# Kernel tuning notes

Measured on AMD Instinct MI355X. Metric: run time of the kernel, lower is better.

## Reference

```python
import jax, jax.numpy as jnp
import numpy as np

H = 512          # hidden_size
B, S, L = 32, 2048, 2
D = 2 * H        # encoder output / hidden feature dim


def setup_inputs() -> dict:
    key = jax.random.key(0)
    ks = jax.random.split(key, 9)
    lim1 = 1.0 / np.sqrt(D)
    limv = 1.0 / np.sqrt(H)
    return {
        "hidden": jax.random.normal(ks[0], (L, B, D), jnp.float32),
        "encoder_outputs": jax.random.normal(ks[1], (B, S, D), jnp.float32),
        "mask": jax.random.randint(ks[2], (B, S), 0, 2, jnp.int32),
        "W1_w": jax.random.uniform(ks[3], (H, D), jnp.float32, -lim1, lim1),
        "W1_b": jax.random.uniform(ks[4], (H,), jnp.float32, -lim1, lim1),
        "W2_w": jax.random.uniform(ks[5], (H, D), jnp.float32, -lim1, lim1),
        "W2_b": jax.random.uniform(ks[6], (H,), jnp.float32, -lim1, lim1),
        "V_w": jax.random.uniform(ks[7], (1, H), jnp.float32, -limv, limv),
        "V_b": jax.random.uniform(ks[8], (1,), jnp.float32, -limv, limv),
    }


def reference(hidden, encoder_outputs, mask, W1_w, W1_b, W2_w, W2_b, V_w, V_b):
    # query: last layer hidden state, broadcast over sequence -> [B, 1, D]
    query = hidden[-1][:, None, :]
    # W1(enc) + W2(query): [B, S, H]
    proj = (jnp.einsum('bsd,hd->bsh', encoder_outputs, W1_w) + W1_b
            + jnp.einsum('bqd,hd->bqh', query, W2_w) + W2_b)
    # V projection -> scores [B, S]
    score = jnp.einsum('bsh,h->bs', jnp.tanh(proj), V_w[0]) + V_b[0]
    score = jnp.where(mask == 0, jnp.float32(-1e9), score)
    attn_weights = jax.nn.softmax(score, axis=1)          # [B, S]
    context = jnp.einsum('bs,bsd->bd', attn_weights, encoder_outputs)  # [B, D]
    return context, attn_weights
```

## Files before the change

kernel.cpp:

```cpp
#include <hip/hip_runtime.h>
#include <hip/hip_bf16.h>

#define B_ 32
#define S_ 2048
#define D_ 1024
#define H_ 512
#define M_ (B_*S_)
#define BM 128
#define BN 128
#define BK 64

typedef __attribute__((ext_vector_type(8))) short short8;
typedef __attribute__((ext_vector_type(4))) float f32x4;

__device__ __forceinline__ unsigned short f2bf(float f){
  unsigned u = __builtin_bit_cast(unsigned, f);
  u += 0x7FFFu + ((u>>16)&1u);
  return (unsigned short)(u>>16);
}

__device__ __forceinline__ int swz(int row, int kshort){
  return row*BK + ((kshort & 56) ^ ((row&7)<<3)) + (kshort & 7);
}

__global__ __launch_bounds__(256) void convw_kernel(
    const float* __restrict__ W1, unsigned short* __restrict__ W1s){
  int tid = blockIdx.x*256 + threadIdx.x;
  int n = tid*8;
  int h = n >> 10;
  int k = n & 1023;
  int bn = h >> 7, row = h & 127;
  int kt = k >> 6, kk = k & 63;
  float4 lo = *(const float4*)(W1 + n);
  float4 hi = *(const float4*)(W1 + n + 4);
  short8 r;
  r[0]=(short)f2bf(lo.x); r[1]=(short)f2bf(lo.y); r[2]=(short)f2bf(lo.z); r[3]=(short)f2bf(lo.w);
  r[4]=(short)f2bf(hi.x); r[5]=(short)f2bf(hi.y); r[6]=(short)f2bf(hi.z); r[7]=(short)f2bf(hi.w);
  *(short8*)&W1s[(bn*16 + kt)*(BN*BK) + swz(row, kk)] = r;
}

__global__ __launch_bounds__(256) void qbias_kernel(
    const float* __restrict__ hidden, const float* __restrict__ W2,
    const float* __restrict__ W1b, const float* __restrict__ W2b,
    float* __restrict__ qb){
  int b = blockIdx.x, h0 = blockIdx.y*64;
  int wave = threadIdx.x>>6, lane = threadIdx.x&63;
  const float* q = hidden + (size_t)(B_ + b)*D_;
  for (int i=0;i<16;i++){
    int h = h0 + wave*16 + i;
    const float* w = W2 + (size_t)h*D_;
    float s = 0.f;
    #pragma unroll
    for (int it=0; it<4; ++it){
      int d = it*256 + lane*4;
      const float4 qq = *(const float4*)(q+d);
      const float4 ww = *(const float4*)(w+d);
      s += qq.x*ww.x + qq.y*ww.y + qq.z*ww.z + qq.w*ww.w;
    }
    #pragma unroll
    for (int off=1; off<64; off<<=1) s += __shfl_xor(s, off);
    if (lane==0) qb[b*H_ + h] = s + W1b[h] + W2b[h];
  }
}

__global__ __launch_bounds__(256, 2) void score_gemm(
    const float* __restrict__ enc, const unsigned short* __restrict__ W1s,
    const float* __restrict__ qb, const float* __restrict__ Vw,
    float* __restrict__ score_p){
  const int id  = blockIdx.x;
  const int xcd = id & 7;
  const int j   = id >> 3;
  const int bm  = xcd*64 + (j >> 2);
  const int bn  = j & 3;
  const int m0 = bm*BM, h0 = bn*BN;
  const int tid = threadIdx.x, lane = tid&63, wave = tid>>6;
  const int wm = (wave>>1)*64, wn = (wave&1)*64;

  __shared__ __align__(16) unsigned short As[BM*BK];
  __shared__ __align__(16) unsigned short Bs[BN*BK];

  f32x4 acc[4][4];
  #pragma unroll
  for (int i=0;i<4;i++)
    #pragma unroll
    for (int j2=0;j2<4;j2++)
      acc[i][j2] = (f32x4)(0.f);

  const int arow = tid>>3, akc = (tid&7)*8;

  float4 aLo[4], aHi[4];
  #pragma unroll
  for (int i=0;i<4;i++){
    int c = tid + i*256;
    int row = c>>3, kc = (c&7)*8;
    const float4* pa = (const float4*)(enc + (size_t)(m0+row)*D_ + kc);
    aLo[i]=pa[0]; aHi[i]=pa[1];
  }

  for (int kt=0; kt<16; ++kt){
    __builtin_amdgcn_s_barrier();
    __builtin_amdgcn_sched_barrier(0);
    const unsigned short* bsrc = W1s + (bn*16 + kt)*(BN*BK);
    #pragma unroll
    for (int i=0;i<4;i++){
      __builtin_amdgcn_global_load_lds(
        (const __attribute__((address_space(1))) unsigned int*)(bsrc + i*2048 + tid*8),
        (__attribute__((address_space(3))) unsigned int*)&Bs[i*2048 + tid*8],
        16, 0, 0);
    }
    __builtin_amdgcn_sched_barrier(0);
    #pragma unroll
    for (int i=0;i<4;i++){
      int c = tid + i*256;
      int row = c>>3, kc = (c&7)*8;
      short8 av;
      av[0]=(short)f2bf(aLo[i].x); av[1]=(short)f2bf(aLo[i].y);
      av[2]=(short)f2bf(aLo[i].z); av[3]=(short)f2bf(aLo[i].w);
      av[4]=(short)f2bf(aHi[i].x); av[5]=(short)f2bf(aHi[i].y);
      av[6]=(short)f2bf(aHi[i].z); av[7]=(short)f2bf(aHi[i].w);
      *(short8*)&As[swz(row, kc)] = av;
    }
    if (kt < 15){
      const int kk1 = (kt+1)*BK;
      #pragma unroll
      for (int i=0;i<4;i++){
        int c = tid + i*256;
        int row = c>>3, kc = (c&7)*8;
        const float4* pa = (const float4*)(enc + (size_t)(m0+row)*D_ + kk1 + kc);
        aLo[i]=pa[0]; aHi[i]=pa[1];
      }
      __builtin_amdgcn_sched_barrier(0);
      asm volatile("s_waitcnt vmcnt(8) lgkmcnt(0)" ::: "memory");
    } else {
      __builtin_amdgcn_sched_barrier(0);
      asm volatile("s_waitcnt vmcnt(0) lgkmcnt(0)" ::: "memory");
    }
    __builtin_amdgcn_s_barrier();
    __builtin_amdgcn_sched_barrier(0);
    #pragma unroll
    for (int kh=0; kh<2; ++kh){
      const int kb = kh*32 + (lane>>4)*8;
      short8 af[4], bf[4];
      #pragma unroll
      for (int mi=0;mi<4;mi++){
        int row = wm + mi*16 + (lane&15);
        af[mi] = *(const short8*)&As[swz(row, kb)];
      }
      #pragma unroll
      for (int ni=0;ni<4;ni++){
        int row = wn + ni*16 + (lane&15);
        bf[ni] = *(const short8*)&Bs[swz(row, kb)];
      }
      #pragma unroll
      for (int mi=0;mi<4;mi++)
        #pragma unroll
        for (int ni=0;ni<4;ni++)
          acc[mi][ni] = __builtin_amdgcn_mfma_f32_16x16x32_bf16(af[mi], bf[ni], acc[mi][ni], 0,0,0);
    }
  }

  const int bidx = m0 >> 11;
  float qv[4], vwv[4];
  #pragma unroll
  for (int ni=0;ni<4;ni++){
    int h = h0 + wn + ni*16 + (lane&15);
    qv[ni]  = qb[bidx*H_ + h];
    vwv[ni] = Vw[h];
  }
  __shared__ float psum[4][BM];
  #pragma unroll
  for (int mi=0;mi<4;mi++){
    #pragma unroll
    for (int r=0;r<4;r++){
      float s = 0.f;
      #pragma unroll
      for (int ni=0;ni<4;ni++) s += tanhf(acc[mi][ni][r] + qv[ni]) * vwv[ni];
      s += __shfl_xor(s,1); s += __shfl_xor(s,2);
      s += __shfl_xor(s,4); s += __shfl_xor(s,8);
      if ((lane&15)==0){
        int m = wm + mi*16 + ((lane>>4)<<2) + r;
        psum[wave][m] = s;
      }
    }
  }
  __syncthreads();
  if (tid < BM){
    int w0 = (tid>>6)*2;
    score_p[(size_t)bn*M_ + m0 + tid] = psum[w0][tid] + psum[w0+1][tid];
  }
}

__global__ __launch_bounds__(256) void softmax_kernel(
    const float* __restrict__ score_p, const int* __restrict__ mask,
    float* __restrict__ attn){
  int b = blockIdx.x, tid = threadIdx.x;
  int wave = tid>>6, lane = tid&63;
  __shared__ float red[8];
  float v[8];
  float mx = -1e30f;
  #pragma unroll
  for (int i=0;i<8;i++){
    int idx = b*S_ + tid + i*256;
    float sc = score_p[idx] + score_p[M_+idx] + score_p[2*M_+idx] + score_p[3*M_+idx];
    v[i] = (mask[idx]==0) ? -1e9f : sc;
    mx = fmaxf(mx, v[i]);
  }
  #pragma unroll
  for (int off=1; off<64; off<<=1) mx = fmaxf(mx, __shfl_xor(mx, off));
  if (lane==0) red[wave] = mx;
  __syncthreads();
  mx = fmaxf(fmaxf(red[0],red[1]), fmaxf(red[2],red[3]));
  float sum = 0.f;
  #pragma unroll
  for (int i=0;i<8;i++){ v[i] = __expf(v[i]-mx); sum += v[i]; }
  #pragma unroll
  for (int off=1; off<64; off<<=1) sum += __shfl_xor(sum, off);
  if (lane==0) red[4+wave] = sum;
  __syncthreads();
  float inv = 1.f/(red[4]+red[5]+red[6]+red[7]);
  #pragma unroll
  for (int i=0;i<8;i++) attn[b*S_ + tid + i*256] = v[i]*inv;
}

__global__ __launch_bounds__(256) void context_kernel(
    const float* __restrict__ enc, const float* __restrict__ attn,
    float* __restrict__ ctx){
  int b = blockIdx.x, sc = blockIdx.y;
  int s0 = sc*64;
  int d4 = threadIdx.x*4;
  const float* ep = enc + ((size_t)b*S_ + s0)*D_ + d4;
  const float* ap = attn + b*S_ + s0;
  float4 a0 = make_float4(0.f,0.f,0.f,0.f);
  float4 a1 = make_float4(0.f,0.f,0.f,0.f);
  #pragma unroll 4
  for (int i=0;i<64;i+=2){
    float w0 = ap[i], w1 = ap[i+1];
    float4 e0 = *(const float4*)(ep + (size_t)i*D_);
    float4 e1 = *(const float4*)(ep + (size_t)(i+1)*D_);
    a0.x = fmaf(w0, e0.x, a0.x); a0.y = fmaf(w0, e0.y, a0.y);
    a0.z = fmaf(w0, e0.z, a0.z); a0.w = fmaf(w0, e0.w, a0.w);
    a1.x = fmaf(w1, e1.x, a1.x); a1.y = fmaf(w1, e1.y, a1.y);
    a1.z = fmaf(w1, e1.z, a1.z); a1.w = fmaf(w1, e1.w, a1.w);
  }
  float* o = ctx + b*D_ + d4;
  atomicAdd(o+0, a0.x+a1.x); atomicAdd(o+1, a0.y+a1.y);
  atomicAdd(o+2, a0.z+a1.z); atomicAdd(o+3, a0.w+a1.w);
}

extern "C" void kernel_launch(void* const* d_in, const int* in_sizes, int n_in,
                              void* d_out, int out_size, void* d_ws, size_t ws_size,
                              hipStream_t stream){
  const float* hidden = (const float*)d_in[0];
  const float* enc    = (const float*)d_in[1];
  const int*   mask   = (const int*)d_in[2];
  const float* W1w    = (const float*)d_in[3];
  const float* W1b    = (const float*)d_in[4];
  const float* W2w    = (const float*)d_in[5];
  const float* W2b    = (const float*)d_in[6];
  const float* Vw     = (const float*)d_in[7];
  float* out = (float*)d_out;

  float* qb           = (float*)d_ws;
  float* score_p      = qb + B_*H_;
  unsigned short* W1s = (unsigned short*)(score_p + 4*M_);

  hipMemsetAsync(out, 0, (size_t)B_*D_*sizeof(float), stream);

  convw_kernel  <<<H_*D_/8/256,     256, 0, stream>>>(W1w, W1s);
  qbias_kernel  <<<dim3(B_, H_/64), 256, 0, stream>>>(hidden, W2w, W1b, W2b, qb);
  score_gemm    <<<4*(M_/BM),       256, 0, stream>>>(enc, W1s, qb, Vw, score_p);
  softmax_kernel<<<B_,              256, 0, stream>>>(score_p, mask, out + B_*D_);
  context_kernel<<<dim3(B_, 32),    256, 0, stream>>>(enc, out + B_*D_, out);
}
```

Baseline: 190.3 us.

## Double-buffer score GEMM LDS, use fast tanh, restructure qbias and context kernels

The score GEMM now keeps two LDS buffers for A and B, so the next tile's loads and bf16 conversion overlap MFMA compute with one barrier per k-step instead of two. tanhf is replaced by an exp/rcp formulation to cut epilogue cost. qbias is reorganised so each W2 row is loaded once and reused across all batches, using fewer blocks. The context kernel uses nontemporal vector loads and four accumulators. The costs are double the LDS for the GEMM and slightly lower tanh accuracy.

```diff
diff --git a/kernel.cpp b/kernel.cpp
--- a/kernel.cpp
+++ b/kernel.cpp
@@ -9,6 +9,7 @@
 #define BM 128
 #define BN 128
 #define BK 64
+#define TILE (BM*BK)
 
 typedef __attribute__((ext_vector_type(8))) short short8;
 typedef __attribute__((ext_vector_type(4))) float f32x4;
@@ -17,6 +18,10 @@
   unsigned u = __builtin_bit_cast(unsigned, f);
   u += 0x7FFFu + ((u>>16)&1u);
   return (unsigned short)(u>>16);
+}
+
+__device__ __forceinline__ float fast_tanh(float x){
+  return 1.f - 2.f*__builtin_amdgcn_rcpf(__expf(2.f*x) + 1.f);
 }
 
 __device__ __forceinline__ int swz(int row, int kshort){
@@ -36,30 +41,34 @@
   short8 r;
   r[0]=(short)f2bf(lo.x); r[1]=(short)f2bf(lo.y); r[2]=(short)f2bf(lo.z); r[3]=(short)f2bf(lo.w);
   r[4]=(short)f2bf(hi.x); r[5]=(short)f2bf(hi.y); r[6]=(short)f2bf(hi.z); r[7]=(short)f2bf(hi.w);
-  *(short8*)&W1s[(bn*16 + kt)*(BN*BK) + swz(row, kk)] = r;
+  *(short8*)&W1s[(bn*16 + kt)*TILE + swz(row, kk)] = r;
 }
 
 __global__ __launch_bounds__(256) void qbias_kernel(
     const float* __restrict__ hidden, const float* __restrict__ W2,
     const float* __restrict__ W1b, const float* __restrict__ W2b,
     float* __restrict__ qb){
-  int b = blockIdx.x, h0 = blockIdx.y*64;
+  int h0 = blockIdx.x*16;
   int wave = threadIdx.x>>6, lane = threadIdx.x&63;
-  const float* q = hidden + (size_t)(B_ + b)*D_;
-  for (int i=0;i<16;i++){
-    int h = h0 + wave*16 + i;
+  for (int r=0;r<4;r++){
+    int h = h0 + wave*4 + r;
     const float* w = W2 + (size_t)h*D_;
-    float s = 0.f;
+    float4 wv[4];
     #pragma unroll
-    for (int it=0; it<4; ++it){
-      int d = it*256 + lane*4;
-      const float4 qq = *(const float4*)(q+d);
-      const float4 ww = *(const float4*)(w+d);
-      s += qq.x*ww.x + qq.y*ww.y + qq.z*ww.z + qq.w*ww.w;
+    for (int it=0;it<4;it++) wv[it] = *(const float4*)(w + it*256 + lane*4);
+    float bias = W1b[h] + W2b[h];
+    for (int b=0;b<B_;b++){
+      const float* q = hidden + (size_t)(B_+b)*D_;
+      float s = 0.f;
+      #pragma unroll
+      for (int it=0;it<4;it++){
+        float4 qq = *(const float4*)(q + it*256 + lane*4);
+        s += qq.x*wv[it].x + qq.y*wv[it].y + qq.z*wv[it].z + qq.w*wv[it].w;
+      }
+      #pragma unroll
+      for (int off=1; off<64; off<<=1) s += __shfl_xor(s, off);
+      if (lane==0) qb[b*H_ + h] = s + bias;
     }
-    #pragma unroll
-    for (int off=1; off<64; off<<=1) s += __shfl_xor(s, off);
-    if (lane==0) qb[b*H_ + h] = s + W1b[h] + W2b[h];
   }
 }
 
@@ -76,8 +85,8 @@
   const int tid = threadIdx.x, lane = tid&63, wave = tid>>6;
   const int wm = (wave>>1)*64, wn = (wave&1)*64;
 
-  __shared__ __align__(16) unsigned short As[BM*BK];
-  __shared__ __align__(16) unsigned short Bs[BN*BK];
+  __shared__ __align__(16) unsigned short As[2][TILE];
+  __shared__ __align__(16) unsigned short Bs[2][TILE];
 
   f32x4 acc[4][4];
   #pragma unroll
@@ -86,78 +95,65 @@
     for (int j2=0;j2<4;j2++)
       acc[i][j2] = (f32x4)(0.f);
 
-  const int arow = tid>>3, akc = (tid&7)*8;
-
   float4 aLo[4], aHi[4];
-  #pragma unroll
-  for (int i=0;i<4;i++){
-    int c = tid + i*256;
-    int row = c>>3, kc = (c&7)*8;
-    const float4* pa = (const float4*)(enc + (size_t)(m0+row)*D_ + kc);
-    aLo[i]=pa[0]; aHi[i]=pa[1];
-  }
-
-  for (int kt=0; kt<16; ++kt){
+
+#define LOAD_A(KT) do{ const int kkx=(KT)*BK; \
+  _Pragma("unroll") for (int i=0;i<4;i++){ \
+    int c=tid+i*256; int row=c>>3, kc=(c&7)*8; \
+    const float4* pa=(const float4*)(enc+(size_t)(m0+row)*D_+kkx+kc); \
+    aLo[i]=pa[0]; aHi[i]=pa[1]; } }while(0)
+
+#define GLD_B(KT,P) do{ const unsigned short* bsrc=W1s+(size_t)(bn*16+(KT))*TILE; \
+  _Pragma("unroll") for (int i=0;i<4;i++){ \
+    __builtin_amdgcn_global_load_lds( \
+      (const __attribute__((address_space(1))) unsigned int*)(bsrc+i*2048+tid*8), \
+      (__attribute__((address_space(3))) unsigned int*)&Bs[P][i*2048+tid*8], 16,0,0); } }while(0)
+
+#define CVT_A(P) do{ \
+  _Pragma("unroll") for (int i=0;i<4;i++){ \
+    int c=tid+i*256; int row=c>>3, kc=(c&7)*8; short8 av; \
+    av[0]=(short)f2bf(aLo[i].x); av[1]=(short)f2bf(aLo[i].y); \
+    av[2]=(short)f2bf(aLo[i].z); av[3]=(short)f2bf(aLo[i].w); \
+    av[4]=(short)f2bf(aHi[i].x); av[5]=(short)f2bf(aHi[i].y); \
+    av[6]=(short)f2bf(aHi[i].z); av[7]=(short)f2bf(aHi[i].w); \
+    *(short8*)&As[P][swz(row,kc)] = av; } }while(0)
+
+#define COMPUTE(P) do{ \
+  _Pragma("unroll") for (int kh=0; kh<2; ++kh){ \
+    const int kb = kh*32 + (lane>>4)*8; \
+    short8 af[4], bf[4]; \
+    _Pragma("unroll") for (int mi=0;mi<4;mi++){ \
+      int row=wm+mi*16+(lane&15); af[mi]=*(const short8*)&As[P][swz(row,kb)]; } \
+    _Pragma("unroll") for (int ni=0;ni<4;ni++){ \
+      int row=wn+ni*16+(lane&15); bf[ni]=*(const short8*)&Bs[P][swz(row,kb)]; } \
+    _Pragma("unroll") for (int mi=0;mi<4;mi++) \
+      _Pragma("unroll") for (int ni=0;ni<4;ni++) \
+        acc[mi][ni]=__builtin_amdgcn_mfma_f32_16x16x32_bf16(af[mi],bf[ni],acc[mi][ni],0,0,0); \
+  } }while(0)
+
+  LOAD_A(0);
+  GLD_B(0,0);
+  CVT_A(0);
+  LOAD_A(1);
+  asm volatile("s_waitcnt vmcnt(8) lgkmcnt(0)" ::: "memory");
+  __builtin_amdgcn_s_barrier();
+
+  #pragma unroll 2
+  for (int kt=0; kt<14; ++kt){
+    const int p = kt&1;
+    GLD_B(kt+1, p^1);
+    CVT_A(p^1);
+    LOAD_A(kt+2);
+    COMPUTE(p);
+    asm volatile("s_waitcnt vmcnt(8) lgkmcnt(0)" ::: "memory");
     __builtin_amdgcn_s_barrier();
-    __builtin_amdgcn_sched_barrier(0);
-    const unsigned short* bsrc = W1s + (bn*16 + kt)*(BN*BK);
-    #pragma unroll
-    for (int i=0;i<4;i++){
-      __builtin_amdgcn_global_load_lds(
-        (const __attribute__((address_space(1))) unsigned int*)(bsrc + i*2048 + tid*8),
-        (__attribute__((address_space(3))) unsigned int*)&Bs[i*2048 + tid*8],
-        16, 0, 0);
-    }
-    __builtin_amdgcn_sched_barrier(0);
-    #pragma unroll
-    for (int i=0;i<4;i++){
-      int c = tid + i*256;
-      int row = c>>3, kc = (c&7)*8;
-      short8 av;
-      av[0]=(short)f2bf(aLo[i].x); av[1]=(short)f2bf(aLo[i].y);
-      av[2]=(short)f2bf(aLo[i].z); av[3]=(short)f2bf(aLo[i].w);
-      av[4]=(short)f2bf(aHi[i].x); av[5]=(short)f2bf(aHi[i].y);
-      av[6]=(short)f2bf(aHi[i].z); av[7]=(short)f2bf(aHi[i].w);
-      *(short8*)&As[swz(row, kc)] = av;
-    }
-    if (kt < 15){
-      const int kk1 = (kt+1)*BK;
-      #pragma unroll
-      for (int i=0;i<4;i++){
-        int c = tid + i*256;
-        int row = c>>3, kc = (c&7)*8;
-        const float4* pa = (const float4*)(enc + (size_t)(m0+row)*D_ + kk1 + kc);
-        aLo[i]=pa[0]; aHi[i]=pa[1];
-      }
-      __builtin_amdgcn_sched_barrier(0);
-      asm volatile("s_waitcnt vmcnt(8) lgkmcnt(0)" ::: "memory");
-    } else {
-      __builtin_amdgcn_sched_barrier(0);
-      asm volatile("s_waitcnt vmcnt(0) lgkmcnt(0)" ::: "memory");
-    }
-    __builtin_amdgcn_s_barrier();
-    __builtin_amdgcn_sched_barrier(0);
-    #pragma unroll
-    for (int kh=0; kh<2; ++kh){
-      const int kb = kh*32 + (lane>>4)*8;
-      short8 af[4], bf[4];
-      #pragma unroll
-      for (int mi=0;mi<4;mi++){
-        int row = wm + mi*16 + (lane&15);
-        af[mi] = *(const short8*)&As[swz(row, kb)];
-      }
-      #pragma unroll
-      for (int ni=0;ni<4;ni++){
-        int row = wn + ni*16 + (lane&15);
-        bf[ni] = *(const short8*)&Bs[swz(row, kb)];
-      }
-      #pragma unroll
-      for (int mi=0;mi<4;mi++)
-        #pragma unroll
-        for (int ni=0;ni<4;ni++)
-          acc[mi][ni] = __builtin_amdgcn_mfma_f32_16x16x32_bf16(af[mi], bf[ni], acc[mi][ni], 0,0,0);
-    }
-  }
+  }
+  GLD_B(15,1);
+  CVT_A(1);
+  COMPUTE(0);
+  asm volatile("s_waitcnt vmcnt(0) lgkmcnt(0)" ::: "memory");
+  __builtin_amdgcn_s_barrier();
+  COMPUTE(1);
 
   const int bidx = m0 >> 11;
   float qv[4], vwv[4];
@@ -174,7 +170,7 @@
     for (int r=0;r<4;r++){
       float s = 0.f;
       #pragma unroll
-      for (int ni=0;ni<4;ni++) s += tanhf(acc[mi][ni][r] + qv[ni]) * vwv[ni];
+      for (int ni=0;ni<4;ni++) s += fast_tanh(acc[mi][ni][r] + qv[ni]) * vwv[ni];
       s += __shfl_xor(s,1); s += __shfl_xor(s,2);
       s += __shfl_xor(s,4); s += __shfl_xor(s,8);
       if ((lane&15)==0){
@@ -230,21 +226,20 @@
   int d4 = threadIdx.x*4;
   const float* ep = enc + ((size_t)b*S_ + s0)*D_ + d4;
   const float* ap = attn + b*S_ + s0;
-  float4 a0 = make_float4(0.f,0.f,0.f,0.f);
-  float4 a1 = make_float4(0.f,0.f,0.f,0.f);
-  #pragma unroll 4
-  for (int i=0;i<64;i+=2){
-    float w0 = ap[i], w1 = ap[i+1];
-    float4 e0 = *(const float4*)(ep + (size_t)i*D_);
-    float4 e1 = *(const float4*)(ep + (size_t)(i+1)*D_);
-    a0.x = fmaf(w0, e0.x, a0.x); a0.y = fmaf(w0, e0.y, a0.y);
-    a0.z = fmaf(w0, e0.z, a0.z); a0.w = fmaf(w0, e0.w, a0.w);
-    a1.x = fmaf(w1, e1.x, a1.x); a1.y = fmaf(w1, e1.y, a1.y);
-    a1.z = fmaf(w1, e1.z, a1.z); a1.w = fmaf(w1, e1.w, a1.w);
-  }
+  f32x4 a0=(f32x4)(0.f), a1=(f32x4)(0.f), a2=(f32x4)(0.f), a3=(f32x4)(0.f);
+  #pragma unroll 2
+  for (int i=0;i<64;i+=4){
+    f32x4 w = *(const f32x4*)(ap + i);
+    f32x4 e0 = __builtin_nontemporal_load((const f32x4*)(ep + (size_t)i*D_));
+    f32x4 e1 = __builtin_nontemporal_load((const f32x4*)(ep + (size_t)(i+1)*D_));
+    f32x4 e2 = __builtin_nontemporal_load((const f32x4*)(ep + (size_t)(i+2)*D_));
+    f32x4 e3 = __builtin_nontemporal_load((const f32x4*)(ep + (size_t)(i+3)*D_));
+    a0 += w[0]*e0; a1 += w[1]*e1; a2 += w[2]*e2; a3 += w[3]*e3;
+  }
+  f32x4 t = (a0+a1) + (a2+a3);
   float* o = ctx + b*D_ + d4;
-  atomicAdd(o+0, a0.x+a1.x); atomicAdd(o+1, a0.y+a1.y);
-  atomicAdd(o+2, a0.z+a1.z); atomicAdd(o+3, a0.w+a1.w);
+  atomicAdd(o+0, t[0]); atomicAdd(o+1, t[1]);
+  atomicAdd(o+2, t[2]); atomicAdd(o+3, t[3]);
 }
 
 extern "C" void kernel_launch(void* const* d_in, const int* in_sizes, int n_in,
@@ -266,9 +261,9 @@
 
   hipMemsetAsync(out, 0, (size_t)B_*D_*sizeof(float), stream);
 
-  convw_kernel  <<<H_*D_/8/256,     256, 0, stream>>>(W1w, W1s);
-  qbias_kernel  <<<dim3(B_, H_/64), 256, 0, stream>>>(hidden, W2w, W1b, W2b, qb);
-  score_gemm    <<<4*(M_/BM),       256, 0, stream>>>(enc, W1s, qb, Vw, score_p);
-  softmax_kernel<<<B_,              256, 0, stream>>>(score_p, mask, out + B_*D_);
-  context_kernel<<<dim3(B_, 32),    256, 0, stream>>>(enc, out + B_*D_, out);
-}
+  convw_kernel  <<<H_*D_/8/256, 256, 0, stream>>>(W1w, W1s);
+  qbias_kernel  <<<H_/16,       256, 0, stream>>>(hidden, W2w, W1b, W2b, qb);
+  score_gemm    <<<4*(M_/BM),   256, 0, stream>>>(enc, W1s, qb, Vw, score_p);
+  softmax_kernel<<<B_,          256, 0, stream>>>(score_p, mask, out + B_*D_);
+  context_kernel<<<dim3(B_,32), 256, 0, stream>>>(enc, out + B_*D_, out);
+}
```

Measured after the change: 249.8 us. 31.2% more time.
